# Kernel optimization log

Measured on AMD Instinct MI355X. Metric: run time of the kernel, lower is better.

## Reference

```python
import jax, jax.numpy as jnp
import numpy as np

B, C_IN, T_IN = 128, 128, 2500
C_OUT, K, STRIDE, PAD = 64, 27, 4, 13  # T_out = 625
BN_EPS = 1e-5
SURROGATE_ALPHA = 4.0


def binarize_weight(w):
    """1-bit (XNOR-Net style) weight quantization with straight-through estimator.
    w: (O, I, K). Per-output-channel scale = mean |w|."""
    alpha = jnp.mean(jnp.abs(w), axis=(1, 2), keepdims=True)
    wq = jnp.sign(w) * alpha
    return w + jax.lax.stop_gradient(wq - w)


def spike(x):
    """Heaviside spike with sigmoid surrogate gradient (STE)."""
    hard = (x > 0).astype(x.dtype)
    soft = jax.nn.sigmoid(SURROGATE_ALPHA * x)
    return soft + jax.lax.stop_gradient(hard - soft)


def setup_inputs() -> dict:
    key = jax.random.key(0)
    ks = jax.random.split(key, 8)
    scale_conv = 1.0 / np.sqrt(C_IN * K)
    scale_lin = 1.0 / np.sqrt(C_OUT)
    return {
        "x": jax.random.normal(ks[0], (B, C_IN, T_IN), dtype=jnp.float32),
        "conv_w": jax.random.normal(ks[1], (C_OUT, C_IN, K), dtype=jnp.float32) * scale_conv,
        "conv_b": jnp.zeros((C_OUT,), dtype=jnp.float32),
        "bn_gamma": jnp.ones((C_OUT,), dtype=jnp.float32),
        "bn_beta": jnp.zeros((C_OUT,), dtype=jnp.float32),
        "bn_mean": jax.random.normal(ks[2], (C_OUT,), dtype=jnp.float32) * 0.1,
        "bn_var": jax.random.uniform(ks[3], (C_OUT,), dtype=jnp.float32, minval=0.5, maxval=1.5),
        "wq": jax.random.normal(ks[4], (C_OUT, C_OUT), dtype=jnp.float32) * scale_lin,
        "wk": jax.random.normal(ks[5], (C_OUT, C_OUT), dtype=jnp.float32) * scale_lin,
        "wv": jax.random.normal(ks[6], (C_OUT, C_OUT), dtype=jnp.float32) * scale_lin,
        "wo": jax.random.normal(ks[7], (C_OUT, C_OUT), dtype=jnp.float32) * scale_lin,
    }


def reference(x, conv_w, conv_b, bn_gamma, bn_beta, bn_mean, bn_var, wq, wk, wv, wo):
    # --- 1-bit quantized conv1d, stride 4 ---
    w_bin = binarize_weight(conv_w)
    y = jax.lax.conv_general_dilated(
        x, w_bin, window_strides=(STRIDE,), padding=[(PAD, PAD)],
        dimension_numbers=("NCH", "OIH", "NCH"))
    y = y + conv_b[None, :, None]  # (B, C_OUT, 625)

    # --- BatchNorm1d (inference stats) + ELU ---
    inv = jax.lax.rsqrt(bn_var + BN_EPS)
    y = (y - bn_mean[None, :, None]) * (inv * bn_gamma)[None, :, None] + bn_beta[None, :, None]
    y = jax.nn.elu(y)

    # --- Global spiking attention (single head) ---
    s = spike(y)                                   # (B, C, T) binary spikes
    q = jnp.einsum("oc,bct->bot", wq, s)           # (B, C, T)
    k = jnp.einsum("oc,bct->bot", wk, s)
    v = jnp.einsum("oc,bct->bot", wv, y)
    scores = jnp.einsum("bct,bcs->bts", q, k) / jnp.sqrt(jnp.asarray(C_OUT, y.dtype))
    attn = jax.nn.softmax(scores, axis=-1)         # (B, T, T)
    ctx = jnp.einsum("bts,bcs->bct", attn, v)      # (B, C, T)
    out = y + jnp.einsum("oc,bct->bot", wo, ctx)   # residual
    return out
```

## Files before the change

### kernel.cpp

```cpp
#include <hip/hip_runtime.h>
#include <math.h>

#define B_    128
#define CIN   128
#define TIN   2500
#define COUT  64
#define KW    27
#define TOUT  625
#define TPAD  640
#define CTT   32
#define GROWS 152

typedef __bf16 bf16x8 __attribute__((ext_vector_type(8)));
typedef float  f32x4  __attribute__((ext_vector_type(4)));

__device__ __forceinline__ unsigned short f32_to_bf16_rne(float v) {
    unsigned u = __float_as_uint(v);
    u += 0x7FFFu + ((u >> 16) & 1u);
    return (unsigned short)(u >> 16);
}

__device__ __forceinline__ f32x4 mfma_bf16(bf16x8 a, bf16x8 b, f32x4 c) {
    return __builtin_amdgcn_mfma_f32_16x16x32_bf16(a, b, c, 0, 0, 0);
}

__global__ void binarize_kernel(const float* __restrict__ w,
                                unsigned* __restrict__ sgn2,
                                float* __restrict__ alpha_out) {
    int o = blockIdx.x, tid = threadIdx.x;
    __shared__ float red[256];
    const float* wo_ = w + (size_t)o * (CIN * KW);
    float s = 0.f;
    for (int idx = tid; idx < CIN * KW; idx += 256) s += fabsf(wo_[idx]);
    red[tid] = s;
    __syncthreads();
    for (int st = 128; st > 0; st >>= 1) {
        if (tid < st) red[tid] += red[tid + st];
        __syncthreads();
    }
    if (tid == 0) alpha_out[o] = red[0] / (float)(CIN * KW);

    for (int t = tid; t < KW * 4; t += 256) {
        int kk = t >> 2, kg = t & 3;
        unsigned u = 0;
#pragma unroll
        for (int cs = 0; cs < 4; cs++) {
#pragma unroll
            for (int j = 0; j < 8; j++) {
                int c = cs * 32 + kg * 8 + j;
                float v = wo_[c * KW + kk];
                unsigned bit = (v > 0.f) ? 0u : 1u;
                u |= bit << (cs * 8 + j);
            }
        }
        sgn2[(kk * 4 + kg) * 64 + o] = u;
    }
}

__global__ void transpose_w_kernel(const float* __restrict__ wq, const float* __restrict__ wk,
                                   const float* __restrict__ wv, const float* __restrict__ wo,
                                   const float* __restrict__ conv_b, const float* __restrict__ gamma_,
                                   const float* __restrict__ beta_, const float* __restrict__ mean_,
                                   const float* __restrict__ var_, const float* __restrict__ alpha_,
                                   float* __restrict__ dstT,
                                   unsigned short* __restrict__ wo_h, unsigned short* __restrict__ wo_l,
                                   float* __restrict__ scA, float* __restrict__ scB) {
    if (blockIdx.x < 3) {
        const float* srcs[3] = {wq, wk, wv};
        const float* src = srcs[blockIdx.x];
        float* dst = dstT + (size_t)blockIdx.x * 4096;
        for (int idx = threadIdx.x; idx < 4096; idx += 256) {
            int o = idx >> 6, c = idx & 63;
            dst[c * 64 + o] = src[idx];
        }
    } else if (blockIdx.x == 3) {
        for (int idx = threadIdx.x; idx < 4096; idx += 256) {
            float v = wo[idx];
            unsigned short h = f32_to_bf16_rne(v);
            float hf = __uint_as_float((unsigned)h << 16);
            wo_h[idx] = h;
            wo_l[idx] = f32_to_bf16_rne(v - hf);
        }
    } else {
        int o = threadIdx.x;
        if (o < 64) {
            float inv = rsqrtf(var_[o] + 1e-5f);
            float G = gamma_[o] * inv;
            scA[o] = alpha_[o] * G;
            scB[o] = (conv_b[o] - mean_[o]) * G + beta_[o];
        }
    }
}

__global__ __launch_bounds__(256, 4) void conv_kernel(
    const float* __restrict__ x, const unsigned* __restrict__ sgn2,
    const float* __restrict__ scA, const float* __restrict__ scB,
    float* __restrict__ y_out)
{
    __shared__ __align__(16) unsigned short xhi[GROWS * 128];
    __shared__ __align__(16) unsigned long long sgnlut[16];

    int b = blockIdx.y;
    int t0 = blockIdx.x * CTT;
    int tid = threadIdx.x;

    if (tid < 16) {
        unsigned long long e = 0;
#pragma unroll
        for (int j = 0; j < 4; ++j) {
            unsigned long long h = ((tid >> j) & 1) ? 0xBF80ull : 0x3F80ull;
            e |= h << (16 * j);
        }
        sgnlut[tid] = e;
    }

    const float* xb = x + (size_t)b * CIN * TIN;
    int gbase = 4 * t0 - 13;
    for (int task = tid; task < 16 * GROWS; task += 256) {
        int c8 = task / GROWS, gl = task - c8 * GROWS;
        int g = gbase + gl;
        bool valid = (gl < 151) && ((unsigned)g < (unsigned)TIN);
        float vs[8];
#pragma unroll
        for (int j = 0; j < 8; j++)
            vs[j] = valid ? xb[(size_t)(c8 * 8 + j) * TIN + g] : 0.f;
        union { unsigned u[4]; uint4 q; } H;
#pragma unroll
        for (int j = 0; j < 4; j++) {
            unsigned short h0 = f32_to_bf16_rne(vs[2 * j]);
            unsigned short h1 = f32_to_bf16_rne(vs[2 * j + 1]);
            H.u[j] = (unsigned)h0 | ((unsigned)h1 << 16);
        }
        int c8p = c8 ^ ((gl >> 2) & 15);
        *(uint4*)(xhi + gl * 128 + c8p * 8) = H.q;
    }
    __syncthreads();

    int wave = tid >> 6, lane = tid & 63;
    int o0 = wave * 16;
    int n = lane & 15, kg = lane >> 4;

    f32x4 acc0 = {0.f, 0.f, 0.f, 0.f};
    f32x4 acc1 = {0.f, 0.f, 0.f, 0.f};

    const unsigned* sgb = sgn2 + (size_t)kg * 64 + o0 + n;
    unsigned sa = sgb[0];

#pragma unroll 1
    for (int kk = 0; kk < KW; ++kk) {
        unsigned na = 0;
        if (kk < KW - 1) na = sgb[(kk + 1) * 256];
        int gl = 4 * n + kk;
        int rot = (gl >> 2) & 15;
        const unsigned short* xr0 = xhi + gl * 128;
        const unsigned short* xr1 = xr0 + 8192;
#pragma unroll
        for (int cs = 0; cs < 4; ++cs) {
            int c8p = (cs * 4 + kg) ^ rot;
            bf16x8 b0 = *(const bf16x8*)(xr0 + c8p * 8);
            bf16x8 b1 = *(const bf16x8*)(xr1 + c8p * 8);
            unsigned byte = (sa >> (8 * cs)) & 0xFFu;
            union { unsigned long long u[2]; bf16x8 v; } A;
            A.u[0] = sgnlut[byte & 15u];
            A.u[1] = sgnlut[byte >> 4];
            acc0 = mfma_bf16(A.v, b0, acc0);
            acc1 = mfma_bf16(A.v, b1, acc1);
        }
        sa = na;
    }

    int quad = lane >> 4, col = lane & 15;
#pragma unroll
    for (int tt = 0; tt < 2; ++tt) {
        int t_g = t0 + tt * 16 + col;
        if (t_g < TOUT) {
            f32x4 a = tt ? acc1 : acc0;
#pragma unroll
            for (int r = 0; r < 4; ++r) {
                int o = o0 + quad * 4 + r;
                float s = a[r] * scA[o] + scB[o];
                float yv = s > 0.f ? s : expm1f(s);
                y_out[((size_t)b * COUT + o) * TOUT + t_g] = yv;
            }
        }
    }
}

__global__ __launch_bounds__(256, 2) void proj_kernel(
    const float* __restrict__ y, const float* __restrict__ wqT,
    const float* __restrict__ wkT, const float* __restrict__ wvT,
    unsigned short* __restrict__ q_h, unsigned short* __restrict__ k_h,
    unsigned short* __restrict__ vT_h)
{
    __shared__ float w_sh[3 * 4096];
    __shared__ __align__(16) float y_sh[64 * 72];
    int b = blockIdx.y, t0 = blockIdx.x * 64, tid = threadIdx.x;

    for (int i = tid; i < 4096; i += 256) {
        w_sh[i]         = wqT[i];
        w_sh[4096 + i]  = wkT[i];
        w_sh[8192 + i]  = wvT[i];
    }
    const float* yb = y + (size_t)b * COUT * TOUT;
    for (int i = tid; i < 64 * 64; i += 256) {
        int c = i >> 6, tt = i & 63;
        int t = t0 + tt;
        y_sh[c * 72 + tt] = (t < TOUT) ? yb[c * TOUT + t] : 0.f;
    }
    __syncthreads();

    int oo = tid & 63, tq = tid >> 6;
    float q[16], k[16], v[16];
#pragma unroll
    for (int j = 0; j < 16; j++) { q[j] = 0.f; k[j] = 0.f; v[j] = 0.f; }

#pragma unroll 1
    for (int c = 0; c < 64; ++c) {
        float wq = w_sh[c * 64 + oo];
        float wk = w_sh[4096 + c * 64 + oo];
        float wv = w_sh[8192 + c * 64 + oo];
        const float* yr = &y_sh[c * 72 + tq * 16];
#pragma unroll
        for (int j4 = 0; j4 < 4; ++j4) {
            float4 y4 = *(const float4*)(yr + 4 * j4);
            float ys[4] = {y4.x, y4.y, y4.z, y4.w};
#pragma unroll
            for (int j = 0; j < 4; ++j) {
                float yv = ys[j];
                float sp = yv > 0.f ? 1.f : 0.f;
                q[4 * j4 + j] += wq * sp;
                k[4 * j4 + j] += wk * sp;
                v[4 * j4 + j] += wv * yv;
            }
        }
    }

    int tbase = t0 + tq * 16;
#pragma unroll
    for (int j = 0; j < 16; ++j) {
        size_t off = ((size_t)b * TPAD + tbase + j) * 64 + oo;
        q_h[off] = f32_to_bf16_rne(q[j]);
        k_h[off] = f32_to_bf16_rne(k[j]);
    }
    union { unsigned short u[16]; uint4 q4[2]; } V;
#pragma unroll
    for (int j = 0; j < 16; ++j) V.u[j] = f32_to_bf16_rne(v[j]);
    unsigned short* vp = vT_h + ((size_t)b * 64 + oo) * TPAD + tbase;
    ((uint4*)vp)[0] = V.q4[0];
    ((uint4*)vp)[1] = V.q4[1];
}

__global__ __launch_bounds__(512, 3) void attn_kernel(
    const unsigned short* __restrict__ q_h, const unsigned short* __restrict__ k_h,
    const unsigned short* __restrict__ vT_h, const float* __restrict__ y,
    const unsigned short* __restrict__ wo_h, const unsigned short* __restrict__ wo_l,
    float* __restrict__ out)
{
    __shared__ __align__(16) float sc_sh[16 * 648];
    __shared__ float ctx_sh[2 * 64 * 17];
    __shared__ float rden[16];

    int b = blockIdx.y, t0 = blockIdx.x * 16, tid = threadIdx.x;
    int wave = tid >> 6, lane = tid & 63;
    int quad = lane >> 4, nlo = lane & 15;

    const unsigned short* qb = q_h + ((size_t)b * TPAD + t0 + nlo) * 64 + quad * 8;
    bf16x8 qa0 = *(const bf16x8*)(qb);
    bf16x8 qa1 = *(const bf16x8*)(qb + 32);
    const unsigned short* kbase = k_h + (size_t)b * TPAD * 64 + quad * 8;
#pragma unroll 5
    for (int nt = 0; nt < 5; ++nt) {
        int s = wave * 80 + nt * 16 + nlo;
        const unsigned short* krow = kbase + (size_t)s * 64;
        bf16x8 kb0 = *(const bf16x8*)(krow);
        bf16x8 kb1 = *(const bf16x8*)(krow + 32);
        f32x4 acc = {0.f, 0.f, 0.f, 0.f};
        acc = mfma_bf16(qa0, kb0, acc);
        acc = mfma_bf16(qa1, kb1, acc);
#pragma unroll
        for (int r = 0; r < 4; ++r)
            sc_sh[(quad * 4 + r) * 648 + s] = acc[r] * 0.125f;
    }
    __syncthreads();

    int ti1 = tid >> 5, sg = tid & 31;
    float* srow = &sc_sh[ti1 * 648];
    float mx = -3.0e38f;
    for (int s = sg; s < TOUT; s += 32) mx = fmaxf(mx, srow[s]);
#pragma unroll
    for (int off = 16; off >= 1; off >>= 1) mx = fmaxf(mx, __shfl_xor(mx, off));

    unsigned short* prow = (unsigned short*)srow;
    float sum = 0.f;
#pragma unroll
    for (int k2 = 0; k2 < 10; ++k2) {
        int s = 2 * sg + 64 * k2;
        float2 v2 = *(const float2*)(srow + s);
        float e0 = (s     < TOUT) ? __expf(v2.x - mx) : 0.f;
        float e1 = (s + 1 < TOUT) ? __expf(v2.y - mx) : 0.f;
        sum += e0 + e1;
        unsigned u0 = __float_as_uint(e0); u0 += 0x7FFFu + ((u0 >> 16) & 1u);
        unsigned u1 = __float_as_uint(e1); u1 += 0x7FFFu + ((u1 >> 16) & 1u);
        *(unsigned*)(prow + s) = (u0 >> 16) | (u1 & 0xFFFF0000u);
    }
#pragma unroll
    for (int off = 16; off >= 1; off >>= 1) sum += __shfl_xor(sum, off);
    if (sg == 0) rden[ti1] = 1.f / sum;
    __syncthreads();

    int cw = (wave & 3) * 16, kh = wave >> 2;
    const unsigned short* vb = vT_h + ((size_t)b * 64 + cw + nlo) * TPAD;
    const unsigned short* pb = (const unsigned short*)sc_sh + nlo * 1296;
    f32x4 cacc = {0.f, 0.f, 0.f, 0.f};
    int ks0 = kh * 10;
#pragma unroll 5
    for (int i = 0; i < 10; ++i) {
        int ks = ks0 + i;
        bf16x8 pv = *(const bf16x8*)(pb + ks * 32 + quad * 8);
        bf16x8 v8 = *(const bf16x8*)(vb + ks * 32 + quad * 8);
        cacc = mfma_bf16(pv, v8, cacc);
    }
#pragma unroll
    for (int r = 0; r < 4; ++r)
        ctx_sh[kh * 1088 + (cw + nlo) * 17 + quad * 4 + r] = cacc[r] * rden[quad * 4 + r];
    __syncthreads();

    if (wave < 4) {
        const unsigned short* woh = wo_h + (size_t)(wave * 16 + nlo) * 64 + quad * 8;
        const unsigned short* wol = wo_l + (size_t)(wave * 16 + nlo) * 64 + quad * 8;
        f32x4 oacc = {0.f, 0.f, 0.f, 0.f};
#pragma unroll
        for (int ks = 0; ks < 2; ++ks) {
            union { unsigned short u[8]; bf16x8 v; } Bc;
#pragma unroll
            for (int j = 0; j < 8; ++j) {
                int c = ks * 32 + quad * 8 + j;
                float cv = ctx_sh[c * 17 + nlo] + ctx_sh[1088 + c * 17 + nlo];
                Bc.u[j] = f32_to_bf16_rne(cv);
            }
            bf16x8 ah = *(const bf16x8*)(woh + ks * 32);
            bf16x8 al = *(const bf16x8*)(wol + ks * 32);
            oacc = mfma_bf16(ah, Bc.v, oacc);
            oacc = mfma_bf16(al, Bc.v, oacc);
        }
        int t_g = t0 + nlo;
        if (t_g < TOUT) {
#pragma unroll
            for (int r = 0; r < 4; ++r) {
                int o = wave * 16 + quad * 4 + r;
                size_t off = ((size_t)b * COUT + o) * TOUT + t_g;
                out[off] = y[off] + oacc[r];
            }
        }
    }
}

extern "C" void kernel_launch(void* const* d_in, const int* in_sizes, int n_in,
                              void* d_out, int out_size, void* d_ws, size_t ws_size,
                              hipStream_t stream) {
    const float* x        = (const float*)d_in[0];
    const float* conv_w   = (const float*)d_in[1];
    const float* conv_b   = (const float*)d_in[2];
    const float* bn_gamma = (const float*)d_in[3];
    const float* bn_beta  = (const float*)d_in[4];
    const float* bn_mean  = (const float*)d_in[5];
    const float* bn_var   = (const float*)d_in[6];
    const float* wq       = (const float*)d_in[7];
    const float* wk       = (const float*)d_in[8];
    const float* wv       = (const float*)d_in[9];
    const float* wo       = (const float*)d_in[10];
    float* out = (float*)d_out;
    float* ws  = (float*)d_ws;

    unsigned* sgn2        = (unsigned*)ws;
    float* alpha          = ws + 110592;
    float* scA            = ws + 110656;
    float* scB            = ws + 110720;
    float* wT4            = ws + 110848;
    unsigned short* wo_h  = (unsigned short*)(ws + 123136);
    unsigned short* wo_l  = (unsigned short*)(ws + 125184);
    float* yb             = ws + 131072;
    unsigned short* q_h   = (unsigned short*)(ws + 5251072);
    unsigned short* k_h   = (unsigned short*)(ws + 7872512);
    unsigned short* vT_h  = (unsigned short*)(ws + 10493952);

    hipLaunchKernelGGL(binarize_kernel, dim3(64), dim3(256), 0, stream, conv_w, sgn2, alpha);
    hipLaunchKernelGGL(transpose_w_kernel, dim3(5), dim3(256), 0, stream,
                       wq, wk, wv, wo, conv_b, bn_gamma, bn_beta, bn_mean, bn_var, alpha,
                       wT4, wo_h, wo_l, scA, scB);
    hipLaunchKernelGGL(conv_kernel, dim3(20, 128), dim3(256), 0, stream,
                       x, sgn2, scA, scB, yb);
    hipLaunchKernelGGL(proj_kernel, dim3(10, 128), dim3(256), 0, stream,
                       yb, wT4, wT4 + 4096, wT4 + 8192, q_h, k_h, vT_h);
    hipLaunchKernelGGL(attn_kernel, dim3(40, 128), dim3(512), 0, stream,
                       q_h, k_h, vT_h, yb, wo_h, wo_l, out);
}
```

Baseline: 478.2 us.

## Fuse Q/K/V projection into conv epilogue using split-bf16 MFMA

Removes the separate proj_kernel and computes the Q, K and V projections in the conv kernel epilogue. The post-ELU y tile and its spikes are staged in swizzled shared memory, then multiplied by bf16 hi/lo-split weights with MFMA instead of FP32 FMAs. This avoids re-reading y from global memory and one kernel launch. In exchange the conv kernel gets extra epilogue work, syncs and register pressure, and y is rounded to bf16 before the V product, which adds precision risk.

```diff
diff --git a/kernel.cpp b/kernel.cpp
--- a/kernel.cpp
+++ b/kernel.cpp
@@ -62,16 +62,20 @@
                                    const float* __restrict__ conv_b, const float* __restrict__ gamma_,
                                    const float* __restrict__ beta_, const float* __restrict__ mean_,
                                    const float* __restrict__ var_, const float* __restrict__ alpha_,
-                                   float* __restrict__ dstT,
+                                   unsigned short* __restrict__ w3_h, unsigned short* __restrict__ w3_l,
                                    unsigned short* __restrict__ wo_h, unsigned short* __restrict__ wo_l,
                                    float* __restrict__ scA, float* __restrict__ scB) {
     if (blockIdx.x < 3) {
         const float* srcs[3] = {wq, wk, wv};
         const float* src = srcs[blockIdx.x];
-        float* dst = dstT + (size_t)blockIdx.x * 4096;
+        unsigned short* dh = w3_h + (size_t)blockIdx.x * 4096;
+        unsigned short* dl = w3_l + (size_t)blockIdx.x * 4096;
         for (int idx = threadIdx.x; idx < 4096; idx += 256) {
-            int o = idx >> 6, c = idx & 63;
-            dst[c * 64 + o] = src[idx];
+            float v = src[idx];
+            unsigned short h = f32_to_bf16_rne(v);
+            float hf = __uint_as_float((unsigned)h << 16);
+            dh[idx] = h;
+            dl[idx] = f32_to_bf16_rne(v - hf);
         }
     } else if (blockIdx.x == 3) {
         for (int idx = threadIdx.x; idx < 4096; idx += 256) {
@@ -95,10 +99,18 @@
 __global__ __launch_bounds__(256, 4) void conv_kernel(
     const float* __restrict__ x, const unsigned* __restrict__ sgn2,
     const float* __restrict__ scA, const float* __restrict__ scB,
-    float* __restrict__ y_out)
+    const unsigned short* __restrict__ w3_h, const unsigned short* __restrict__ w3_l,
+    float* __restrict__ y_out,
+    unsigned short* __restrict__ q_h, unsigned short* __restrict__ k_h,
+    unsigned short* __restrict__ vT_h)
 {
     __shared__ __align__(16) unsigned short xhi[GROWS * 128];
     __shared__ __align__(16) unsigned long long sgnlut[16];
+    unsigned short* y_sh = xhi;
+    unsigned short* s_sh = xhi + 2048;
+    unsigned short* q_sh = xhi + 4096;
+    unsigned short* k_sh = xhi + 6144;
+    unsigned short* v_sh = xhi + 8192;
 
     int b = blockIdx.y;
     int t0 = blockIdx.x * CTT;
@@ -169,85 +181,109 @@
         sa = na;
     }
 
-    int quad = lane >> 4, col = lane & 15;
+    int quad = kg, col = n;
+    unsigned long long ypk[2], spk[2];
 #pragma unroll
     for (int tt = 0; tt < 2; ++tt) {
         int t_g = t0 + tt * 16 + col;
-        if (t_g < TOUT) {
-            f32x4 a = tt ? acc1 : acc0;
-#pragma unroll
-            for (int r = 0; r < 4; ++r) {
-                int o = o0 + quad * 4 + r;
-                float s = a[r] * scA[o] + scB[o];
-                float yv = s > 0.f ? s : expm1f(s);
+        f32x4 a = tt ? acc1 : acc0;
+        unsigned long long yp = 0, sp = 0;
+#pragma unroll
+        for (int r = 0; r < 4; ++r) {
+            int o = o0 + quad * 4 + r;
+            float s = a[r] * scA[o] + scB[o];
+            float yv = s > 0.f ? s : expm1f(s);
+            if (t_g < TOUT) {
                 y_out[((size_t)b * COUT + o) * TOUT + t_g] = yv;
+                yp |= (unsigned long long)f32_to_bf16_rne(yv) << (16 * r);
+                if (yv > 0.f) sp |= 0x3F80ull << (16 * r);
             }
         }
-    }
-}
-
-__global__ __launch_bounds__(256, 2) void proj_kernel(
-    const float* __restrict__ y, const float* __restrict__ wqT,
-    const float* __restrict__ wkT, const float* __restrict__ wvT,
-    unsigned short* __restrict__ q_h, unsigned short* __restrict__ k_h,
-    unsigned short* __restrict__ vT_h)
-{
-    __shared__ float w_sh[3 * 4096];
-    __shared__ __align__(16) float y_sh[64 * 72];
-    int b = blockIdx.y, t0 = blockIdx.x * 64, tid = threadIdx.x;
-
-    for (int i = tid; i < 4096; i += 256) {
-        w_sh[i]         = wqT[i];
-        w_sh[4096 + i]  = wkT[i];
-        w_sh[8192 + i]  = wvT[i];
-    }
-    const float* yb = y + (size_t)b * COUT * TOUT;
-    for (int i = tid; i < 64 * 64; i += 256) {
-        int c = i >> 6, tt = i & 63;
-        int t = t0 + tt;
-        y_sh[c * 72 + tt] = (t < TOUT) ? yb[c * TOUT + t] : 0.f;
-    }
-    __syncthreads();
-
-    int oo = tid & 63, tq = tid >> 6;
-    float q[16], k[16], v[16];
-#pragma unroll
-    for (int j = 0; j < 16; j++) { q[j] = 0.f; k[j] = 0.f; v[j] = 0.f; }
-
-#pragma unroll 1
-    for (int c = 0; c < 64; ++c) {
-        float wq = w_sh[c * 64 + oo];
-        float wk = w_sh[4096 + c * 64 + oo];
-        float wv = w_sh[8192 + c * 64 + oo];
-        const float* yr = &y_sh[c * 72 + tq * 16];
-#pragma unroll
-        for (int j4 = 0; j4 < 4; ++j4) {
-            float4 y4 = *(const float4*)(yr + 4 * j4);
-            float ys[4] = {y4.x, y4.y, y4.z, y4.w};
-#pragma unroll
-            for (int j = 0; j < 4; ++j) {
-                float yv = ys[j];
-                float sp = yv > 0.f ? 1.f : 0.f;
-                q[4 * j4 + j] += wq * sp;
-                k[4 * j4 + j] += wk * sp;
-                v[4 * j4 + j] += wv * yv;
-            }
-        }
-    }
-
-    int tbase = t0 + tq * 16;
-#pragma unroll
-    for (int j = 0; j < 16; ++j) {
-        size_t off = ((size_t)b * TPAD + tbase + j) * 64 + oo;
-        q_h[off] = f32_to_bf16_rne(q[j]);
-        k_h[off] = f32_to_bf16_rne(k[j]);
-    }
-    union { unsigned short u[16]; uint4 q4[2]; } V;
-#pragma unroll
-    for (int j = 0; j < 16; ++j) V.u[j] = f32_to_bf16_rne(v[j]);
-    unsigned short* vp = vT_h + ((size_t)b * 64 + oo) * TPAD + tbase;
-    ((uint4*)vp)[0] = V.q4[0];
-    ((uint4*)vp)[1] = V.q4[1];
+        ypk[tt] = yp; spk[tt] = sp;
+    }
+    __syncthreads();
+
+    int c8w = (o0 >> 3) + (quad >> 1);
+    int cof = (quad & 1) * 4;
+#pragma unroll
+    for (int tt = 0; tt < 2; ++tt) {
+        int tl = tt * 16 + col;
+        int idx = tl * 64 + ((c8w ^ (tl & 7)) << 3) + cof;
+        *(unsigned long long*)(y_sh + idx) = ypk[tt];
+        *(unsigned long long*)(s_sh + idx) = spk[tt];
+    }
+    __syncthreads();
+
+    bf16x8 sf[2][2], yf[2][2];
+#pragma unroll
+    for (int tt = 0; tt < 2; ++tt)
+#pragma unroll
+        for (int ks = 0; ks < 2; ++ks) {
+            int tl = tt * 16 + col;
+            int idx = tl * 64 + (((ks * 4 + quad) ^ (tl & 7)) << 3);
+            sf[tt][ks] = *(const bf16x8*)(s_sh + idx);
+            yf[tt][ks] = *(const bf16x8*)(y_sh + idx);
+        }
+    size_t wofs = (size_t)(o0 + col) * 64 + quad * 8;
+    f32x4 qa[2], ka[2], va[2];
+#pragma unroll
+    for (int tt = 0; tt < 2; ++tt) {
+        qa[tt] = (f32x4){0.f, 0.f, 0.f, 0.f};
+        ka[tt] = (f32x4){0.f, 0.f, 0.f, 0.f};
+        va[tt] = (f32x4){0.f, 0.f, 0.f, 0.f};
+    }
+#pragma unroll
+    for (int ks = 0; ks < 2; ++ks) {
+        bf16x8 aqh = *(const bf16x8*)(w3_h + wofs + ks * 32);
+        bf16x8 aql = *(const bf16x8*)(w3_l + wofs + ks * 32);
+        bf16x8 akh = *(const bf16x8*)(w3_h + 4096 + wofs + ks * 32);
+        bf16x8 akl = *(const bf16x8*)(w3_l + 4096 + wofs + ks * 32);
+        bf16x8 avh = *(const bf16x8*)(w3_h + 8192 + wofs + ks * 32);
+        bf16x8 avl = *(const bf16x8*)(w3_l + 8192 + wofs + ks * 32);
+#pragma unroll
+        for (int tt = 0; tt < 2; ++tt) {
+            qa[tt] = mfma_bf16(aqh, sf[tt][ks], qa[tt]);
+            qa[tt] = mfma_bf16(aql, sf[tt][ks], qa[tt]);
+            ka[tt] = mfma_bf16(akh, sf[tt][ks], ka[tt]);
+            ka[tt] = mfma_bf16(akl, sf[tt][ks], ka[tt]);
+            va[tt] = mfma_bf16(avh, yf[tt][ks], va[tt]);
+            va[tt] = mfma_bf16(avl, yf[tt][ks], va[tt]);
+        }
+    }
+#pragma unroll
+    for (int tt = 0; tt < 2; ++tt) {
+        int tl = tt * 16 + col;
+        int idx = tl * 64 + ((c8w ^ (tl & 7)) << 3) + cof;
+        unsigned long long qp = 0, kp = 0;
+#pragma unroll
+        for (int r = 0; r < 4; ++r) {
+            qp |= (unsigned long long)f32_to_bf16_rne(qa[tt][r]) << (16 * r);
+            kp |= (unsigned long long)f32_to_bf16_rne(ka[tt][r]) << (16 * r);
+        }
+        *(unsigned long long*)(q_sh + idx) = qp;
+        *(unsigned long long*)(k_sh + idx) = kp;
+#pragma unroll
+        for (int r = 0; r < 4; ++r) {
+            int c = o0 + quad * 4 + r;
+            int vidx = c * 32 + (((tt * 2 + (col >> 3)) ^ quad) << 3) + (col & 7);
+            v_sh[vidx] = f32_to_bf16_rne(va[tt][r]);
+        }
+    }
+    __syncthreads();
+
+    {
+        int tl = tid >> 3, seg = tid & 7;
+        int idx = tl * 64 + ((seg ^ (tl & 7)) << 3);
+        uint4 qv = *(const uint4*)(q_sh + idx);
+        uint4 kv = *(const uint4*)(k_sh + idx);
+        size_t go = ((size_t)b * TPAD + t0 + tl) * 64 + seg * 8;
+        *(uint4*)(q_h + go) = qv;
+        *(uint4*)(k_h + go) = kv;
+        int c = tid >> 2, ts = tid & 3;
+        int vidx = c * 32 + ((ts ^ ((c >> 2) & 3)) << 3);
+        uint4 vv = *(const uint4*)(v_sh + vidx);
+        *(uint4*)(vT_h + ((size_t)b * 64 + c) * TPAD + t0 + ts * 8) = vv;
+    }
 }
 
 __global__ __launch_bounds__(512, 3) void attn_kernel(
@@ -376,7 +412,8 @@
     float* alpha          = ws + 110592;
     float* scA            = ws + 110656;
     float* scB            = ws + 110720;
-    float* wT4            = ws + 110848;
+    unsigned short* w3_h  = (unsigned short*)(ws + 110848);
+    unsigned short* w3_l  = (unsigned short*)(ws + 116992);
     unsigned short* wo_h  = (unsigned short*)(ws + 123136);
     unsigned short* wo_l  = (unsigned short*)(ws + 125184);
     float* yb             = ws + 131072;
@@ -387,11 +424,9 @@
     hipLaunchKernelGGL(binarize_kernel, dim3(64), dim3(256), 0, stream, conv_w, sgn2, alpha);
     hipLaunchKernelGGL(transpose_w_kernel, dim3(5), dim3(256), 0, stream,
                        wq, wk, wv, wo, conv_b, bn_gamma, bn_beta, bn_mean, bn_var, alpha,
-                       wT4, wo_h, wo_l, scA, scB);
+                       w3_h, w3_l, wo_h, wo_l, scA, scB);
     hipLaunchKernelGGL(conv_kernel, dim3(20, 128), dim3(256), 0, stream,
-                       x, sgn2, scA, scB, yb);
-    hipLaunchKernelGGL(proj_kernel, dim3(10, 128), dim3(256), 0, stream,
-                       yb, wT4, wT4 + 4096, wT4 + 8192, q_h, k_h, vT_h);
+                       x, sgn2, scA, scB, w3_h, w3_l, yb, q_h, k_h, vT_h);
     hipLaunchKernelGGL(attn_kernel, dim3(40, 128), dim3(512), 0, stream,
                        q_h, k_h, vT_h, yb, wo_h, wo_l, out);
 }
```

Measured after the change: 433.0 us. 1.1x faster.
